# Optimization experiments

Measured on AMD Instinct MI355X. Metric: run time of the kernel, lower is better.

## Reference

```python
import jax, jax.numpy as jnp
import numpy as np

B, T, D_IN, H, C = 256, 2048, 64, 32, 16
RHO, SPARSITY = 0.9, 0.1


def _reservoir(rng, n):
    # uniform(-1,1), scale to spectral radius RHO, then sparsify (same order as torch code)
    W = rng.uniform(-1.0, 1.0, (n, n)).astype(np.float32)
    W *= RHO / np.max(np.abs(np.linalg.eigvals(W)))
    W *= (rng.random((n, n)) < SPARSITY).astype(np.float32)
    return jnp.asarray(W)


def _linear(rng, fan_in, fan_out):
    bound = 1.0 / np.sqrt(fan_in)
    W = rng.uniform(-bound, bound, (fan_out, fan_in)).astype(np.float32)
    b = rng.uniform(-bound, bound, (fan_out,)).astype(np.float32)
    return jnp.asarray(W), jnp.asarray(b)


def setup_inputs() -> dict:
    key = jax.random.key(0)
    rng = np.random.default_rng(0)
    x = jax.random.normal(key, (B, T, D_IN), dtype=jnp.float32)
    # frozen encoder input / reservoir weights (uniform(-1,1) weights, default-init biases)
    W_in = jnp.asarray(rng.uniform(-1.0, 1.0, (H, D_IN)).astype(np.float32))
    b_in = jnp.asarray(rng.uniform(-1 / np.sqrt(D_IN), 1 / np.sqrt(D_IN), (H,)).astype(np.float32))
    W_res_enc = _reservoir(rng, H)
    b_res_enc = jnp.asarray(rng.uniform(-1 / np.sqrt(H), 1 / np.sqrt(H), (H,)).astype(np.float32))
    W_code, b_code = _linear(rng, H, C)
    W_co, b_co = _linear(rng, C, H)
    W_res_dec = _reservoir(rng, H)
    b_res_dec = jnp.asarray(rng.uniform(-1 / np.sqrt(H), 1 / np.sqrt(H), (H,)).astype(np.float32))
    W_ro, b_ro = _linear(rng, H, D_IN)
    return dict(x=x, W_in=W_in, b_in=b_in, W_res_enc=W_res_enc, b_res_enc=b_res_enc,
                W_code=W_code, b_code=b_code, W_co=W_co, b_co=b_co,
                W_res_dec=W_res_dec, b_res_dec=b_res_dec, W_ro=W_ro, b_ro=b_ro)


def reference(x, W_in, b_in, W_res_enc, b_res_enc, W_code, b_code, W_co, b_co,
              W_res_dec, b_res_dec, W_ro, b_ro):
    Bs = x.shape[0]
    h0 = jnp.zeros((Bs, W_res_enc.shape[0]), dtype=x.dtype)
    # precompute input projection for all timesteps: [T, B, H]
    u_enc = jnp.swapaxes(jnp.einsum('btd,hd->bth', x, W_in) + b_in, 0, 1)

    def enc_step(h, u):
        h = jnp.tanh(u + h @ W_res_enc.T + b_res_enc)
        return h, h

    _, enc = jax.lax.scan(enc_step, h0, u_enc)
    enc = jnp.swapaxes(enc, 0, 1)                      # [B, T, H]

    z = enc @ W_code.T + b_code                        # [B, T, C]
    h_dec_in = z @ W_co.T + b_co                       # [B, T, H]

    def dec_step(h, u):
        h = jnp.tanh(u + h @ W_res_dec.T + b_res_dec)
        return h, h

    _, dec = jax.lax.scan(dec_step, h0, jnp.swapaxes(h_dec_in, 0, 1))
    dec = jnp.swapaxes(dec, 0, 1)                      # [B, T, H]
    return dec @ W_ro.T + b_ro                         # [B, T, D_IN]
```

## Files before the change

### kernel.cpp

```cpp
#include <hip/hip_runtime.h>
#include <math.h>

#define B_    256
#define T_    2048
#define DIN   64
#define H_    32
#define C_    16

#define CHUNK 256
#define WARM  96
#define NCHUNK (T_ / CHUNK)

#define OFF_WCOMB 0u
#define OFF_BCOMB 4096u
#define OFF_U     (1u << 20)
#define OFF_DEC   ((1u << 20) + (64u << 20))

__device__ __forceinline__ float fast_tanh(float x) {
    float e2 = __expf(x + x);
    return 1.0f - 2.0f * __builtin_amdgcn_rcpf(e2 + 1.0f);
}

__global__ __launch_bounds__(1024) void prep_kernel(
        const float* __restrict__ W_code, const float* __restrict__ b_code,
        const float* __restrict__ W_co,   const float* __restrict__ b_co,
        float* __restrict__ W_comb, float* __restrict__ b_comb) {
    int t = threadIdx.x;
    int i = t >> 5, j = t & 31;
    float s = 0.0f;
#pragma unroll
    for (int c = 0; c < C_; ++c)
        s += W_co[i * C_ + c] * W_code[c * H_ + j];
    W_comb[i * H_ + j] = s;
    if (t < H_) {
        float sb = b_co[t];
#pragma unroll
        for (int c = 0; c < C_; ++c)
            sb += W_co[t * C_ + c] * b_code[c];
        b_comb[t] = sb;
    }
}

__global__ __launch_bounds__(256) void inproj_kernel(
        const float* __restrict__ x, const float* __restrict__ W_in,
        const float* __restrict__ b_in, float* __restrict__ u) {
    __shared__ __align__(16) float lw[H_ * DIN];
    __shared__ float lb[H_];
    for (int v = threadIdx.x; v < H_ * DIN; v += 256) lw[v] = W_in[v];
    if (threadIdx.x < H_) lb[threadIdx.x] = b_in[threadIdx.x];
    __syncthreads();

    long row0 = (long)(blockIdx.x * 256 + threadIdx.x) * 4;
    const float4* xr0 = reinterpret_cast<const float4*>(x + row0 * DIN);
    const float4* xr1 = reinterpret_cast<const float4*>(x + (row0 + 1) * DIN);
    const float4* xr2 = reinterpret_cast<const float4*>(x + (row0 + 2) * DIN);
    const float4* xr3 = reinterpret_cast<const float4*>(x + (row0 + 3) * DIN);
    const float4* lw4 = reinterpret_cast<const float4*>(lw);

    float acc[4][H_];
#pragma unroll
    for (int r = 0; r < 4; ++r)
#pragma unroll
        for (int i = 0; i < H_; ++i) acc[r][i] = 0.0f;

    for (int k4 = 0; k4 < DIN / 4; ++k4) {
        float4 xv0 = xr0[k4], xv1 = xr1[k4], xv2 = xr2[k4], xv3 = xr3[k4];
#pragma unroll
        for (int i = 0; i < H_; ++i) {
            float4 w = lw4[i * (DIN / 4) + k4];
            acc[0][i] += xv0.x * w.x + xv0.y * w.y + xv0.z * w.z + xv0.w * w.w;
            acc[1][i] += xv1.x * w.x + xv1.y * w.y + xv1.z * w.z + xv1.w * w.w;
            acc[2][i] += xv2.x * w.x + xv2.y * w.y + xv2.z * w.z + xv2.w * w.w;
            acc[3][i] += xv3.x * w.x + xv3.y * w.y + xv3.z * w.z + xv3.w * w.w;
        }
    }
#pragma unroll
    for (int r = 0; r < 4; ++r) {
        float4* ur = reinterpret_cast<float4*>(u + (row0 + r) * H_);
#pragma unroll
        for (int q = 0; q < H_ / 4; ++q) {
            float4 o;
            o.x = acc[r][4 * q + 0] + lb[4 * q + 0];
            o.y = acc[r][4 * q + 1] + lb[4 * q + 1];
            o.z = acc[r][4 * q + 2] + lb[4 * q + 2];
            o.w = acc[r][4 * q + 3] + lb[4 * q + 3];
            ur[q] = o;
        }
    }
}

__global__ __launch_bounds__(64) void scan_kernel(
        const float* __restrict__ u,
        const float* __restrict__ W_res_enc, const float* __restrict__ b_res_enc,
        const float* __restrict__ W_res_dec, const float* __restrict__ b_res_dec,
        const float* __restrict__ W_comb,    const float* __restrict__ b_comb,
        float* __restrict__ dec) {
    int lane = threadIdx.x;
    int i = lane & 31;
    int half = lane >> 5;
    int b  = ((blockIdx.x & 127) << 1) | half;
    int c  = blockIdx.x >> 7;
    int t0 = c * CHUNK;
    int tstart = (c == 0) ? 0 : (t0 - WARM);
    int tend = t0 + CHUNK;

    float We[H_], Wc[H_], Wd[H_];
    {
        const float4* we4 = reinterpret_cast<const float4*>(W_res_enc + i * H_);
        const float4* wc4 = reinterpret_cast<const float4*>(W_comb + i * H_);
        const float4* wd4 = reinterpret_cast<const float4*>(W_res_dec + i * H_);
#pragma unroll
        for (int q = 0; q < H_ / 4; ++q) {
            float4 a = we4[q], bq = wc4[q], d = wd4[q];
            We[4*q+0] = a.x;  We[4*q+1] = a.y;  We[4*q+2] = a.z;  We[4*q+3] = a.w;
            Wc[4*q+0] = bq.x; Wc[4*q+1] = bq.y; Wc[4*q+2] = bq.z; Wc[4*q+3] = bq.w;
            Wd[4*q+0] = d.x;  Wd[4*q+1] = d.y;  Wd[4*q+2] = d.z;  Wd[4*q+3] = d.w;
        }
    }
    float be = b_res_enc[i], bc = b_comb[i], bd = b_res_dec[i];

    float henc[H_], hdec[H_];
#pragma unroll
    for (int j = 0; j < H_; ++j) { henc[j] = 0.0f; hdec[j] = 0.0f; }

    __shared__ __align__(16) float lhe[2][H_];
    __shared__ __align__(16) float lhd[2][H_];

    const float* ub = u + ((long)b * T_) * H_ + i;
    float*       db = dec + ((long)b * T_) * H_ + i;

    float ucur = ub[(long)tstart * H_];
    for (int t = tstart; t < tend; ++t) {
        float unext = 0.0f;
        if (t + 1 < tend) unext = ub[(long)(t + 1) * H_];

        float a = ucur + be;
#pragma unroll
        for (int j = 0; j < H_; ++j) a += We[j] * henc[j];
        a = fast_tanh(a);

        lhe[half][i] = a;
#pragma unroll
        for (int q = 0; q < H_ / 4; ++q) {
            float4 v = *reinterpret_cast<const float4*>(&lhe[half][4 * q]);
            henc[4*q+0] = v.x; henc[4*q+1] = v.y;
            henc[4*q+2] = v.z; henc[4*q+3] = v.w;
        }

        float g = bc;
#pragma unroll
        for (int j = 0; j < H_; ++j) g += Wc[j] * henc[j];

        float d = g + bd;
#pragma unroll
        for (int j = 0; j < H_; ++j) d += Wd[j] * hdec[j];
        d = fast_tanh(d);

        lhd[half][i] = d;
#pragma unroll
        for (int q = 0; q < H_ / 4; ++q) {
            float4 v = *reinterpret_cast<const float4*>(&lhd[half][4 * q]);
            hdec[4*q+0] = v.x; hdec[4*q+1] = v.y;
            hdec[4*q+2] = v.z; hdec[4*q+3] = v.w;
        }

        if (t >= t0) db[(long)t * H_] = d;
        ucur = unext;
    }
}

__global__ __launch_bounds__(256) void readout_kernel(
        const float* __restrict__ dec, const float* __restrict__ W_ro,
        const float* __restrict__ b_ro, float* __restrict__ out) {
    __shared__ __align__(16) float lw[DIN * H_];
    __shared__ float lb[DIN];
    for (int v = threadIdx.x; v < DIN * H_; v += 256) lw[v] = W_ro[v];
    if (threadIdx.x < DIN) lb[threadIdx.x] = b_ro[threadIdx.x];
    __syncthreads();

    long row0 = (long)(blockIdx.x * 256 + threadIdx.x) * 2;
    const float4* d0 = reinterpret_cast<const float4*>(dec + row0 * H_);
    const float4* d1 = reinterpret_cast<const float4*>(dec + (row0 + 1) * H_);
    const float4* lw4 = reinterpret_cast<const float4*>(lw);

    float acc[2][DIN];
#pragma unroll
    for (int r = 0; r < 2; ++r)
#pragma unroll
        for (int i = 0; i < DIN; ++i) acc[r][i] = 0.0f;

    for (int k4 = 0; k4 < H_ / 4; ++k4) {
        float4 xv0 = d0[k4], xv1 = d1[k4];
#pragma unroll
        for (int i = 0; i < DIN; ++i) {
            float4 w = lw4[i * (H_ / 4) + k4];
            acc[0][i] += xv0.x * w.x + xv0.y * w.y + xv0.z * w.z + xv0.w * w.w;
            acc[1][i] += xv1.x * w.x + xv1.y * w.y + xv1.z * w.z + xv1.w * w.w;
        }
    }
#pragma unroll
    for (int r = 0; r < 2; ++r) {
        float4* orow = reinterpret_cast<float4*>(out + (row0 + r) * DIN);
#pragma unroll
        for (int q = 0; q < DIN / 4; ++q) {
            float4 o;
            o.x = acc[r][4 * q + 0] + lb[4 * q + 0];
            o.y = acc[r][4 * q + 1] + lb[4 * q + 1];
            o.z = acc[r][4 * q + 2] + lb[4 * q + 2];
            o.w = acc[r][4 * q + 3] + lb[4 * q + 3];
            orow[q] = o;
        }
    }
}

extern "C" void kernel_launch(void* const* d_in, const int* in_sizes, int n_in,
                              void* d_out, int out_size, void* d_ws, size_t ws_size,
                              hipStream_t stream) {
    const float* x         = (const float*)d_in[0];
    const float* W_in      = (const float*)d_in[1];
    const float* b_in      = (const float*)d_in[2];
    const float* W_res_enc = (const float*)d_in[3];
    const float* b_res_enc = (const float*)d_in[4];
    const float* W_code    = (const float*)d_in[5];
    const float* b_code    = (const float*)d_in[6];
    const float* W_co      = (const float*)d_in[7];
    const float* b_co      = (const float*)d_in[8];
    const float* W_res_dec = (const float*)d_in[9];
    const float* b_res_dec = (const float*)d_in[10];
    const float* W_ro      = (const float*)d_in[11];
    const float* b_ro      = (const float*)d_in[12];
    float* out = (float*)d_out;

    char* ws = (char*)d_ws;
    float* W_comb = (float*)(ws + OFF_WCOMB);
    float* b_comb = (float*)(ws + OFF_BCOMB);
    float* u      = (float*)(ws + OFF_U);
    float* decs   = (float*)(ws + OFF_DEC);

    prep_kernel<<<1, 1024, 0, stream>>>(W_code, b_code, W_co, b_co, W_comb, b_comb);
    inproj_kernel<<<(B_ * T_) / (256 * 4), 256, 0, stream>>>(x, W_in, b_in, u);
    scan_kernel<<<(B_ / 2) * NCHUNK, 64, 0, stream>>>(u, W_res_enc, b_res_enc,
                                                      W_res_dec, b_res_dec,
                                                      W_comb, b_comb, decs);
    readout_kernel<<<(B_ * T_) / (256 * 2), 256, 0, stream>>>(decs, W_ro, b_ro, out);
}
```

Measured before the change: 610.2 us.

## Fuse readout projection into scan kernel and restructure input projection

The readout linear layer moves into the scan kernel: each lane computes two output features from the decoder state it already holds and writes them straight to the output. This removes the separate readout kernel and the round trip of the decoder states through global memory. The input projection is rewritten so each lane holds one row of W_in in registers and reads x tiles from LDS, and the dot products in the scan are split into four independent accumulators to shorten dependency chains. In exchange the serial scan loop does more work per step, and register pressure in the scan rises with two extra weight rows.

Measured after the change: 508.0 us. 16.7% less time.

```diff
diff --git a/kernel.cpp b/kernel.cpp
--- a/kernel.cpp
+++ b/kernel.cpp
@@ -14,7 +14,6 @@
 #define OFF_WCOMB 0u
 #define OFF_BCOMB 4096u
 #define OFF_U     (1u << 20)
-#define OFF_DEC   ((1u << 20) + (64u << 20))
 
 __device__ __forceinline__ float fast_tanh(float x) {
     float e2 = __expf(x + x);
@@ -44,57 +43,64 @@
 __global__ __launch_bounds__(256) void inproj_kernel(
         const float* __restrict__ x, const float* __restrict__ W_in,
         const float* __restrict__ b_in, float* __restrict__ u) {
-    __shared__ __align__(16) float lw[H_ * DIN];
-    __shared__ float lb[H_];
-    for (int v = threadIdx.x; v < H_ * DIN; v += 256) lw[v] = W_in[v];
-    if (threadIdx.x < H_) lb[threadIdx.x] = b_in[threadIdx.x];
+    __shared__ __align__(16) float4 lx[128 * 16];
+
+    int tid  = threadIdx.x;
+    int w    = tid >> 6;
+    int lane = tid & 63;
+    int i    = lane & 31;
+    int par  = lane >> 5;
+
+    float Wr[DIN];
+    {
+        const float4* wi4 = reinterpret_cast<const float4*>(W_in + i * DIN);
+#pragma unroll
+        for (int q = 0; q < DIN / 4; ++q) {
+            float4 v = wi4[q];
+            Wr[4*q+0] = v.x; Wr[4*q+1] = v.y; Wr[4*q+2] = v.z; Wr[4*q+3] = v.w;
+        }
+    }
+    float bi = b_in[i];
+
+    long row_base = (long)blockIdx.x * 128;
+    const float4* xg = reinterpret_cast<const float4*>(x) + row_base * 16;
+
+#pragma unroll
+    for (int k = 0; k < 8; ++k)
+        lx[tid + 256 * k] = xg[tid + 256 * k];
     __syncthreads();
 
-    long row0 = (long)(blockIdx.x * 256 + threadIdx.x) * 4;
-    const float4* xr0 = reinterpret_cast<const float4*>(x + row0 * DIN);
-    const float4* xr1 = reinterpret_cast<const float4*>(x + (row0 + 1) * DIN);
-    const float4* xr2 = reinterpret_cast<const float4*>(x + (row0 + 2) * DIN);
-    const float4* xr3 = reinterpret_cast<const float4*>(x + (row0 + 3) * DIN);
-    const float4* lw4 = reinterpret_cast<const float4*>(lw);
-
-    float acc[4][H_];
-#pragma unroll
-    for (int r = 0; r < 4; ++r)
-#pragma unroll
-        for (int i = 0; i < H_; ++i) acc[r][i] = 0.0f;
-
-    for (int k4 = 0; k4 < DIN / 4; ++k4) {
-        float4 xv0 = xr0[k4], xv1 = xr1[k4], xv2 = xr2[k4], xv3 = xr3[k4];
-#pragma unroll
-        for (int i = 0; i < H_; ++i) {
-            float4 w = lw4[i * (DIN / 4) + k4];
-            acc[0][i] += xv0.x * w.x + xv0.y * w.y + xv0.z * w.z + xv0.w * w.w;
-            acc[1][i] += xv1.x * w.x + xv1.y * w.y + xv1.z * w.z + xv1.w * w.w;
-            acc[2][i] += xv2.x * w.x + xv2.y * w.y + xv2.z * w.z + xv2.w * w.w;
-            acc[3][i] += xv3.x * w.x + xv3.y * w.y + xv3.z * w.z + xv3.w * w.w;
-        }
-    }
-#pragma unroll
-    for (int r = 0; r < 4; ++r) {
-        float4* ur = reinterpret_cast<float4*>(u + (row0 + r) * H_);
-#pragma unroll
-        for (int q = 0; q < H_ / 4; ++q) {
-            float4 o;
-            o.x = acc[r][4 * q + 0] + lb[4 * q + 0];
-            o.y = acc[r][4 * q + 1] + lb[4 * q + 1];
-            o.z = acc[r][4 * q + 2] + lb[4 * q + 2];
-            o.w = acc[r][4 * q + 3] + lb[4 * q + 3];
-            ur[q] = o;
-        }
-    }
-}
-
-__global__ __launch_bounds__(64) void scan_kernel(
+#pragma unroll
+    for (int g = 0; g < 4; ++g) {
+        int r0 = w * 32 + g * 8 + par;
+        float acc0 = 0.f, acc1 = 0.f, acc2 = 0.f, acc3 = 0.f;
+#pragma unroll
+        for (int k4 = 0; k4 < 16; ++k4) {
+            float4 wv = { Wr[4*k4+0], Wr[4*k4+1], Wr[4*k4+2], Wr[4*k4+3] };
+            float4 x0 = lx[(r0 + 0) * 16 + k4];
+            float4 x1 = lx[(r0 + 2) * 16 + k4];
+            float4 x2 = lx[(r0 + 4) * 16 + k4];
+            float4 x3 = lx[(r0 + 6) * 16 + k4];
+            acc0 += x0.x * wv.x + x0.y * wv.y + x0.z * wv.z + x0.w * wv.w;
+            acc1 += x1.x * wv.x + x1.y * wv.y + x1.z * wv.z + x1.w * wv.w;
+            acc2 += x2.x * wv.x + x2.y * wv.y + x2.z * wv.z + x2.w * wv.w;
+            acc3 += x3.x * wv.x + x3.y * wv.y + x3.z * wv.z + x3.w * wv.w;
+        }
+        long rg = row_base + r0;
+        u[(rg + 0) * H_ + i] = acc0 + bi;
+        u[(rg + 2) * H_ + i] = acc1 + bi;
+        u[(rg + 4) * H_ + i] = acc2 + bi;
+        u[(rg + 6) * H_ + i] = acc3 + bi;
+    }
+}
+
+__global__ __launch_bounds__(64, 1) void scan_kernel(
         const float* __restrict__ u,
         const float* __restrict__ W_res_enc, const float* __restrict__ b_res_enc,
         const float* __restrict__ W_res_dec, const float* __restrict__ b_res_dec,
         const float* __restrict__ W_comb,    const float* __restrict__ b_comb,
-        float* __restrict__ dec) {
+        const float* __restrict__ W_ro,      const float* __restrict__ b_ro,
+        float* __restrict__ out) {
     int lane = threadIdx.x;
     int i = lane & 31;
     int half = lane >> 5;
@@ -104,20 +110,25 @@
     int tstart = (c == 0) ? 0 : (t0 - WARM);
     int tend = t0 + CHUNK;
 
-    float We[H_], Wc[H_], Wd[H_];
+    float We[H_], Wc[H_], Wd[H_], Wo0[H_], Wo1[H_];
     {
         const float4* we4 = reinterpret_cast<const float4*>(W_res_enc + i * H_);
         const float4* wc4 = reinterpret_cast<const float4*>(W_comb + i * H_);
         const float4* wd4 = reinterpret_cast<const float4*>(W_res_dec + i * H_);
+        const float4* wo0 = reinterpret_cast<const float4*>(W_ro + (2 * i) * H_);
+        const float4* wo1 = reinterpret_cast<const float4*>(W_ro + (2 * i + 1) * H_);
 #pragma unroll
         for (int q = 0; q < H_ / 4; ++q) {
-            float4 a = we4[q], bq = wc4[q], d = wd4[q];
-            We[4*q+0] = a.x;  We[4*q+1] = a.y;  We[4*q+2] = a.z;  We[4*q+3] = a.w;
-            Wc[4*q+0] = bq.x; Wc[4*q+1] = bq.y; Wc[4*q+2] = bq.z; Wc[4*q+3] = bq.w;
-            Wd[4*q+0] = d.x;  Wd[4*q+1] = d.y;  Wd[4*q+2] = d.z;  Wd[4*q+3] = d.w;
+            float4 a = we4[q], bq = wc4[q], d = wd4[q], o0 = wo0[q], o1 = wo1[q];
+            We[4*q+0]=a.x;  We[4*q+1]=a.y;  We[4*q+2]=a.z;  We[4*q+3]=a.w;
+            Wc[4*q+0]=bq.x; Wc[4*q+1]=bq.y; Wc[4*q+2]=bq.z; Wc[4*q+3]=bq.w;
+            Wd[4*q+0]=d.x;  Wd[4*q+1]=d.y;  Wd[4*q+2]=d.z;  Wd[4*q+3]=d.w;
+            Wo0[4*q+0]=o0.x;Wo0[4*q+1]=o0.y;Wo0[4*q+2]=o0.z;Wo0[4*q+3]=o0.w;
+            Wo1[4*q+0]=o1.x;Wo1[4*q+1]=o1.y;Wo1[4*q+2]=o1.z;Wo1[4*q+3]=o1.w;
         }
     }
     float be = b_res_enc[i], bc = b_comb[i], bd = b_res_dec[i];
+    float bo0 = b_ro[2 * i], bo1 = b_ro[2 * i + 1];
 
     float henc[H_], hdec[H_];
 #pragma unroll
@@ -127,17 +138,22 @@
     __shared__ __align__(16) float lhd[2][H_];
 
     const float* ub = u + ((long)b * T_) * H_ + i;
-    float*       db = dec + ((long)b * T_) * H_ + i;
+    float*       ob = out + ((long)b * T_) * DIN + 2 * i;
 
     float ucur = ub[(long)tstart * H_];
     for (int t = tstart; t < tend; ++t) {
         float unext = 0.0f;
         if (t + 1 < tend) unext = ub[(long)(t + 1) * H_];
 
-        float a = ucur + be;
-#pragma unroll
-        for (int j = 0; j < H_; ++j) a += We[j] * henc[j];
-        a = fast_tanh(a);
+        float a0 = ucur + be, a1 = 0.f, a2 = 0.f, a3 = 0.f;
+#pragma unroll
+        for (int j = 0; j < H_; j += 4) {
+            a0 += We[j+0] * henc[j+0];
+            a1 += We[j+1] * henc[j+1];
+            a2 += We[j+2] * henc[j+2];
+            a3 += We[j+3] * henc[j+3];
+        }
+        float a = fast_tanh((a0 + a1) + (a2 + a3));
 
         lhe[half][i] = a;
 #pragma unroll
@@ -147,14 +163,23 @@
             henc[4*q+2] = v.z; henc[4*q+3] = v.w;
         }
 
-        float g = bc;
-#pragma unroll
-        for (int j = 0; j < H_; ++j) g += Wc[j] * henc[j];
-
-        float d = g + bd;
-#pragma unroll
-        for (int j = 0; j < H_; ++j) d += Wd[j] * hdec[j];
-        d = fast_tanh(d);
+        float g0 = bc + bd, g1 = 0.f, g2 = 0.f, g3 = 0.f;
+#pragma unroll
+        for (int j = 0; j < H_; j += 4) {
+            g0 += Wc[j+0] * henc[j+0];
+            g1 += Wc[j+1] * henc[j+1];
+            g2 += Wc[j+2] * henc[j+2];
+            g3 += Wc[j+3] * henc[j+3];
+        }
+        float d0 = 0.f, d1 = 0.f, d2 = 0.f, d3 = 0.f;
+#pragma unroll
+        for (int j = 0; j < H_; j += 4) {
+            d0 += Wd[j+0] * hdec[j+0];
+            d1 += Wd[j+1] * hdec[j+1];
+            d2 += Wd[j+2] * hdec[j+2];
+            d3 += Wd[j+3] * hdec[j+3];
+        }
+        float d = fast_tanh(((g0 + g1) + (g2 + g3)) + ((d0 + d1) + (d2 + d3)));
 
         lhd[half][i] = d;
 #pragma unroll
@@ -164,52 +189,19 @@
             hdec[4*q+2] = v.z; hdec[4*q+3] = v.w;
         }
 
-        if (t >= t0) db[(long)t * H_] = d;
+        if (t >= t0) {
+            float s00 = bo0, s01 = 0.f, s10 = bo1, s11 = 0.f;
+#pragma unroll
+            for (int j = 0; j < H_; j += 2) {
+                s00 += Wo0[j]     * hdec[j];
+                s01 += Wo0[j + 1] * hdec[j + 1];
+                s10 += Wo1[j]     * hdec[j];
+                s11 += Wo1[j + 1] * hdec[j + 1];
+            }
+            float2 o = make_float2(s00 + s01, s10 + s11);
+            *reinterpret_cast<float2*>(ob + (long)t * DIN) = o;
+        }
         ucur = unext;
-    }
-}
-
-__global__ __launch_bounds__(256) void readout_kernel(
-        const float* __restrict__ dec, const float* __restrict__ W_ro,
-        const float* __restrict__ b_ro, float* __restrict__ out) {
-    __shared__ __align__(16) float lw[DIN * H_];
-    __shared__ float lb[DIN];
-    for (int v = threadIdx.x; v < DIN * H_; v += 256) lw[v] = W_ro[v];
-    if (threadIdx.x < DIN) lb[threadIdx.x] = b_ro[threadIdx.x];
-    __syncthreads();
-
-    long row0 = (long)(blockIdx.x * 256 + threadIdx.x) * 2;
-    const float4* d0 = reinterpret_cast<const float4*>(dec + row0 * H_);
-    const float4* d1 = reinterpret_cast<const float4*>(dec + (row0 + 1) * H_);
-    const float4* lw4 = reinterpret_cast<const float4*>(lw);
-
-    float acc[2][DIN];
-#pragma unroll
-    for (int r = 0; r < 2; ++r)
-#pragma unroll
-        for (int i = 0; i < DIN; ++i) acc[r][i] = 0.0f;
-
-    for (int k4 = 0; k4 < H_ / 4; ++k4) {
-        float4 xv0 = d0[k4], xv1 = d1[k4];
-#pragma unroll
-        for (int i = 0; i < DIN; ++i) {
-            float4 w = lw4[i * (H_ / 4) + k4];
-            acc[0][i] += xv0.x * w.x + xv0.y * w.y + xv0.z * w.z + xv0.w * w.w;
-            acc[1][i] += xv1.x * w.x + xv1.y * w.y + xv1.z * w.z + xv1.w * w.w;
-        }
-    }
-#pragma unroll
-    for (int r = 0; r < 2; ++r) {
-        float4* orow = reinterpret_cast<float4*>(out + (row0 + r) * DIN);
-#pragma unroll
-        for (int q = 0; q < DIN / 4; ++q) {
-            float4 o;
-            o.x = acc[r][4 * q + 0] + lb[4 * q + 0];
-            o.y = acc[r][4 * q + 1] + lb[4 * q + 1];
-            o.z = acc[r][4 * q + 2] + lb[4 * q + 2];
-            o.w = acc[r][4 * q + 3] + lb[4 * q + 3];
-            orow[q] = o;
-        }
     }
 }
 
@@ -235,12 +227,10 @@
     float* W_comb = (float*)(ws + OFF_WCOMB);
     float* b_comb = (float*)(ws + OFF_BCOMB);
     float* u      = (float*)(ws + OFF_U);
-    float* decs   = (float*)(ws + OFF_DEC);
 
     prep_kernel<<<1, 1024, 0, stream>>>(W_code, b_code, W_co, b_co, W_comb, b_comb);
-    inproj_kernel<<<(B_ * T_) / (256 * 4), 256, 0, stream>>>(x, W_in, b_in, u);
+    inproj_kernel<<<(B_ * T_) / 128, 256, 0, stream>>>(x, W_in, b_in, u);
     scan_kernel<<<(B_ / 2) * NCHUNK, 64, 0, stream>>>(u, W_res_enc, b_res_enc,
                                                       W_res_dec, b_res_dec,
-                                                      W_comb, b_comb, decs);
-    readout_kernel<<<(B_ * T_) / (256 * 2), 256, 0, stream>>>(decs, W_ro, b_ro, out);
-}
+                                                      W_comb, b_comb, W_ro, b_ro, out);
+}
```
